# Kernel optimization log

Measured on AMD Instinct MI355X. Metric: run time of the kernel, lower is better.

The kernel has to match this reference:

```python
import jax, jax.numpy as jnp
import numpy as np

D = 256        # node/edge feature dim
H = 256        # MLP hidden dim
NG = 80000     # grid (src) nodes
NM = 20000     # mesh (dst) nodes
E = 160000     # g2m edges
EPS = 1e-5


def _mlp(x, W1, b1, W2, b2, g, beta):
    # MeshGraphMLP with hidden_layers=1: Linear -> SiLU -> Linear -> LayerNorm
    h = jax.nn.silu(x @ W1 + b1)
    y = h @ W2 + b2
    mu = jnp.mean(y, axis=-1, keepdims=True)
    var = jnp.var(y, axis=-1, keepdims=True)
    return (y - mu) * jax.lax.rsqrt(var + EPS) * g + beta


def setup_inputs() -> dict:
    key = jax.random.key(0)
    ks = jax.random.split(key, 16)

    def rn(k, shape, s=0.02):
        return jax.random.normal(k, shape, dtype=jnp.float32) * s

    inp = {
        "g2m_efeat": jax.random.normal(ks[0], (E, D), dtype=jnp.float32),
        "grid_nfeat": jax.random.normal(ks[1], (NG, D), dtype=jnp.float32),
        "mesh_nfeat": jax.random.normal(ks[2], (NM, D), dtype=jnp.float32),
        "src_idx": jax.random.randint(ks[3], (E,), 0, NG, dtype=jnp.int32),
        "dst_idx": jax.random.randint(ks[4], (E,), 0, NM, dtype=jnp.int32),
        # edge MLP (concat variant): input = [efeat | src_feat | dst_feat] -> 3D
        "eW1": rn(ks[5], (3 * D, H)), "eb1": jnp.zeros((H,), jnp.float32),
        "eW2": rn(ks[6], (H, D)),     "eb2": jnp.zeros((D,), jnp.float32),
        "eg": jnp.ones((D,), jnp.float32), "ebeta": jnp.zeros((D,), jnp.float32),
        # src node MLP: D -> H -> D
        "sW1": rn(ks[7], (D, H)), "sb1": jnp.zeros((H,), jnp.float32),
        "sW2": rn(ks[8], (H, D)), "sb2": jnp.zeros((D,), jnp.float32),
        "sg": jnp.ones((D,), jnp.float32), "sbeta": jnp.zeros((D,), jnp.float32),
        # dst node MLP: (D_agg + D_node) = 2D -> H -> D
        "dW1": rn(ks[9], (2 * D, H)), "db1": jnp.zeros((H,), jnp.float32),
        "dW2": rn(ks[10], (H, D)),    "db2": jnp.zeros((D,), jnp.float32),
        "dg": jnp.ones((D,), jnp.float32), "dbeta": jnp.zeros((D,), jnp.float32),
    }
    return inp


def reference(g2m_efeat, grid_nfeat, mesh_nfeat, src_idx, dst_idx,
              eW1, eb1, eW2, eb2, eg, ebeta,
              sW1, sb1, sW2, sb2, sg, sbeta,
              dW1, db1, dW2, db2, dg, dbeta):
    # edge MLP: gather src/dst node features, concat with edge features
    e_in = jnp.concatenate(
        [g2m_efeat, grid_nfeat[src_idx], mesh_nfeat[dst_idx]], axis=-1)  # [E, 3D]
    efeat = _mlp(e_in, eW1, eb1, eW2, eb2, eg, ebeta)                    # [E, D]
    # aggregate_and_concat: copy_e_sum scatter to dst mesh nodes, concat node feats
    agg = jax.ops.segment_sum(efeat, dst_idx, num_segments=NM)           # [NM, D]
    cat_feat = jnp.concatenate([agg, mesh_nfeat], axis=-1)               # [NM, 2D]
    mesh_out = mesh_nfeat + _mlp(cat_feat, dW1, db1, dW2, db2, dg, dbeta)
    grid_out = grid_nfeat + _mlp(grid_nfeat, sW1, sb1, sW2, sb2, sg, sbeta)
    return (grid_out, mesh_out)
```

## Files before the change

### kernel.cpp

```cpp
#include <hip/hip_runtime.h>
#include <hip/hip_bf16.h>

#define DD 256
#define NGN 80000
#define NMN 20000
#define NEE 160000

typedef unsigned short u16;
typedef __attribute__((ext_vector_type(8))) short s16x8;
typedef __attribute__((ext_vector_type(4))) short s16x4;
typedef __attribute__((ext_vector_type(4))) float f32x4;

__device__ __forceinline__ u16 f2bf(float f) {
  union { float f; unsigned u; } v; v.f = f;
  unsigned r = (v.u + 0x7FFFu + ((v.u >> 16) & 1u)) >> 16;
  return (u16)r;
}

__global__ void pack_weights(const float* __restrict__ W, u16* __restrict__ dst, int K) {
  int idx = blockIdx.x * 256 + threadIdx.x;
  if (idx >= K * 256) return;
  int i = idx & 7;
  int lane = (idx >> 3) & 63;
  int nt = (idx >> 9) & 15;
  int kt = idx >> 13;
  int k = kt * 32 + 4 * (lane >> 4) + (i < 4 ? i : 12 + i);
  int n = nt * 16 + (lane & 15);
  dst[idx] = f2bf(W[(size_t)k * 256 + n]);
}

__device__ __forceinline__ void stage16k(const u16* __restrict__ gsrc, u16* lds, int tid) {
  const s16x8* s = (const s16x8*)gsrc;
  s16x8* d = (s16x8*)lds;
#pragma unroll
  for (int j = 0; j < 4; ++j) d[tid + 256 * j] = s[tid + 256 * j];
}

template <int MODE, int K1>
__global__ __launch_bounds__(256, 2) void mlp_fused(
    const float* __restrict__ xa, const float* __restrict__ xb,
    const float* __restrict__ xc,
    const int* __restrict__ sidx, const int* __restrict__ didx,
    const u16* __restrict__ W1p, const float* __restrict__ b1,
    const u16* __restrict__ W2p, const float* __restrict__ b2,
    const float* __restrict__ gam, const float* __restrict__ bet,
    const float* __restrict__ resid, float* __restrict__ out, int nrows) {
  __shared__ u16 bstage[8192];
  __shared__ u16 hbuf[64 * 256];
  __shared__ float2 pstats[64][2];

  const int tid = threadIdx.x;
  const int lane = tid & 63;
  const int wave = tid >> 6;
  const int mr = wave >> 1, nc = wave & 1;
  const int g = lane >> 4, lr = lane & 15;
  const int row0 = blockIdx.x * 64;

  const float* pA[2][3];
#pragma unroll
  for (int mt = 0; mt < 2; ++mt) {
    int r = row0 + mr * 32 + mt * 16 + lr;
    if (MODE == 2) r = min(r, nrows - 1);
    pA[mt][0] = xa + (size_t)r * DD;
    if constexpr (MODE == 0) {
      pA[mt][1] = xb + (size_t)sidx[r] * DD;
      pA[mt][2] = xc + (size_t)didx[r] * DD;
    } else if constexpr (MODE == 2) {
      pA[mt][1] = xb + (size_t)r * DD;
    }
  }

  const f32x4 fz = {0.f, 0.f, 0.f, 0.f};
  f32x4 acc[2][8];
#pragma unroll
  for (int mt = 0; mt < 2; ++mt)
#pragma unroll
    for (int nt = 0; nt < 8; ++nt) acc[mt][nt] = fz;

#pragma unroll
  for (int region = 0; region < K1 / 256; ++region) {
    for (int kl = 0; kl < 8; ++kl) {
      const int kt = region * 8 + kl;
      __syncthreads();
      stage16k(W1p + (size_t)kt * 8192, bstage, tid);
      __syncthreads();
      s16x8 afr[2];
      const int c0 = kl * 32 + 4 * g;
#pragma unroll
      for (int mt = 0; mt < 2; ++mt) {
        const float* p = pA[mt][region] + c0;
        f32x4 f0 = *(const f32x4*)p;
        f32x4 f1 = *(const f32x4*)(p + 16);
        s16x8 a;
#pragma unroll
        for (int j = 0; j < 4; ++j) {
          a[j] = (short)f2bf(f0[j]);
          a[4 + j] = (short)f2bf(f1[j]);
        }
        afr[mt] = a;
      }
#pragma unroll
      for (int nt = 0; nt < 8; ++nt) {
        s16x8 b = *(const s16x8*)(bstage + ((size_t)(nc * 8 + nt) * 64 + lane) * 8);
        acc[0][nt] = __builtin_amdgcn_mfma_f32_16x16x32_bf16(afr[0], b, acc[0][nt], 0, 0, 0);
        acc[1][nt] = __builtin_amdgcn_mfma_f32_16x16x32_bf16(afr[1], b, acc[1][nt], 0, 0, 0);
      }
    }
  }

  {
    float b1v[8];
#pragma unroll
    for (int nt = 0; nt < 8; ++nt) b1v[nt] = b1[nc * 128 + nt * 16 + lr];
#pragma unroll
    for (int mt = 0; mt < 2; ++mt)
#pragma unroll
      for (int nt = 0; nt < 8; ++nt)
#pragma unroll
        for (int i = 0; i < 4; ++i) {
          float x = acc[mt][nt][i] + b1v[nt];
          float h = x / (1.f + __expf(-x));
          int rowL = mr * 32 + mt * 16 + 4 * g + i;
          int col = nc * 128 + nt * 16 + lr;
          int byte = rowL * 512 + ((col * 2) ^ ((rowL & 7) << 4));
          *(u16*)((char*)hbuf + byte) = f2bf(h);
        }
  }

  f32x4 acc2[2][8];
#pragma unroll
  for (int mt = 0; mt < 2; ++mt)
#pragma unroll
    for (int nt = 0; nt < 8; ++nt) acc2[mt][nt] = fz;

  for (int kt2 = 0; kt2 < 8; ++kt2) {
    __syncthreads();
    stage16k(W2p + (size_t)kt2 * 8192, bstage, tid);
    __syncthreads();
    s16x8 afr[2];
#pragma unroll
    for (int mt = 0; mt < 2; ++mt) {
      int rowL = mr * 32 + mt * 16 + lr;
      int swz = (rowL & 7) << 4;
      int cL = kt2 * 32 + 4 * g;
      s16x4 lo = *(const s16x4*)((char*)hbuf + rowL * 512 + ((cL * 2) ^ swz));
      s16x4 hi = *(const s16x4*)((char*)hbuf + rowL * 512 + (((cL + 16) * 2) ^ swz));
      s16x8 a;
#pragma unroll
      for (int j = 0; j < 4; ++j) {
        a[j] = lo[j];
        a[4 + j] = hi[j];
      }
      afr[mt] = a;
    }
#pragma unroll
    for (int nt = 0; nt < 8; ++nt) {
      s16x8 b = *(const s16x8*)(bstage + ((size_t)(nc * 8 + nt) * 64 + lane) * 8);
      acc2[0][nt] = __builtin_amdgcn_mfma_f32_16x16x32_bf16(afr[0], b, acc2[0][nt], 0, 0, 0);
      acc2[1][nt] = __builtin_amdgcn_mfma_f32_16x16x32_bf16(afr[1], b, acc2[1][nt], 0, 0, 0);
    }
  }

  float b2v[8], gv[8], bv[8];
#pragma unroll
  for (int nt = 0; nt < 8; ++nt) {
    int col = nc * 128 + nt * 16 + lr;
    b2v[nt] = b2[col];
    gv[nt] = gam[col];
    bv[nt] = bet[col];
  }
#pragma unroll
  for (int mt = 0; mt < 2; ++mt)
#pragma unroll
    for (int i = 0; i < 4; ++i) {
      float s = 0.f, s2 = 0.f;
#pragma unroll
      for (int nt = 0; nt < 8; ++nt) {
        float y = acc2[mt][nt][i] + b2v[nt];
        s += y;
        s2 += y * y;
      }
#pragma unroll
      for (int m = 1; m < 16; m <<= 1) {
        s += __shfl_xor(s, m);
        s2 += __shfl_xor(s2, m);
      }
      if (lr == 0) pstats[mr * 32 + mt * 16 + 4 * g + i][nc] = make_float2(s, s2);
    }
  __syncthreads();
#pragma unroll
  for (int mt = 0; mt < 2; ++mt)
#pragma unroll
    for (int i = 0; i < 4; ++i) {
      int rowL = mr * 32 + mt * 16 + 4 * g + i;
      float2 pa = pstats[rowL][0], pb = pstats[rowL][1];
      float sum = pa.x + pb.x, sq = pa.y + pb.y;
      float mu = sum * (1.f / 256.f);
      float var = fmaxf(sq * (1.f / 256.f) - mu * mu, 0.f);
      float rs = rsqrtf(var + 1e-5f);
      int rg = row0 + rowL;
      if (MODE == 2 && rg >= nrows) continue;
      int dn = 0;
      if constexpr (MODE == 0) dn = didx[rg];
#pragma unroll
      for (int nt = 0; nt < 8; ++nt) {
        int col = nc * 128 + nt * 16 + lr;
        float y = acc2[mt][nt][i] + b2v[nt];
        float val = (y - mu) * rs * gv[nt] + bv[nt];
        if constexpr (MODE == 0) {
          atomicAdd(out + (size_t)dn * DD + col, val);
        } else {
          out[(size_t)rg * DD + col] = resid[(size_t)rg * DD + col] + val;
        }
      }
    }
}

extern "C" void kernel_launch(void* const* d_in, const int* in_sizes, int n_in,
                              void* d_out, int out_size, void* d_ws, size_t ws_size,
                              hipStream_t stream) {
  const float* g2m  = (const float*)d_in[0];
  const float* grid = (const float*)d_in[1];
  const float* mesh = (const float*)d_in[2];
  const int* sidx = (const int*)d_in[3];
  const int* didx = (const int*)d_in[4];
  const float* eW1 = (const float*)d_in[5];
  const float* eb1 = (const float*)d_in[6];
  const float* eW2 = (const float*)d_in[7];
  const float* eb2 = (const float*)d_in[8];
  const float* eg  = (const float*)d_in[9];
  const float* ebt = (const float*)d_in[10];
  const float* sW1 = (const float*)d_in[11];
  const float* sb1 = (const float*)d_in[12];
  const float* sW2 = (const float*)d_in[13];
  const float* sb2 = (const float*)d_in[14];
  const float* sg  = (const float*)d_in[15];
  const float* sbt = (const float*)d_in[16];
  const float* dW1 = (const float*)d_in[17];
  const float* db1 = (const float*)d_in[18];
  const float* dW2 = (const float*)d_in[19];
  const float* db2 = (const float*)d_in[20];
  const float* dg  = (const float*)d_in[21];
  const float* dbt = (const float*)d_in[22];

  float* agg = (float*)d_ws;
  u16* wp = (u16*)((char*)d_ws + (size_t)NMN * DD * 4);
  u16* eW1p = wp;
  u16* eW2p = eW1p + 768 * 256;
  u16* sW1p = eW2p + 256 * 256;
  u16* sW2p = sW1p + 256 * 256;
  u16* dW1p = sW2p + 256 * 256;
  u16* dW2p = dW1p + 512 * 256;

  (void)hipMemsetAsync(agg, 0, (size_t)NMN * DD * 4, stream);
  pack_weights<<<768, 256, 0, stream>>>(eW1, eW1p, 768);
  pack_weights<<<256, 256, 0, stream>>>(eW2, eW2p, 256);
  pack_weights<<<256, 256, 0, stream>>>(sW1, sW1p, 256);
  pack_weights<<<256, 256, 0, stream>>>(sW2, sW2p, 256);
  pack_weights<<<512, 256, 0, stream>>>(dW1, dW1p, 512);
  pack_weights<<<256, 256, 0, stream>>>(dW2, dW2p, 256);

  float* gout = (float*)d_out;
  float* mout = gout + (size_t)NGN * DD;

  mlp_fused<0, 768><<<NEE / 64, 256, 0, stream>>>(
      g2m, grid, mesh, sidx, didx, eW1p, eb1, eW2p, eb2, eg, ebt, nullptr, agg, NEE);
  mlp_fused<1, 256><<<NGN / 64, 256, 0, stream>>>(
      grid, nullptr, nullptr, nullptr, nullptr, sW1p, sb1, sW2p, sb2, sg, sbt, grid, gout, NGN);
  mlp_fused<2, 512><<<(NMN + 63) / 64, 256, 0, stream>>>(
      agg, mesh, nullptr, nullptr, nullptr, dW1p, db1, dW2p, db2, dg, dbt, mesh, mout, NMN);
}
```

Measured before the change: 438.8 us.

## Precompute per-node projections of edge first layer instead of per-edge gathers

Splits the edge MLP's first linear layer by linearity: the grid and mesh node features are each multiplied once by their slice of W1, stored as bf16 in the output buffer as scratch, and then gathered and summed per edge. The edge kernel then only does a K=256 GEMM on edge features on top of the gathered sum, instead of a K=768 GEMM over gathered rows. Kernel order is changed so the mesh and grid MLPs run after the edge kernel and overwrite the scratch. Storing the projections in bf16 adds rounding error, and the gathers now read half-width rows.

```diff
diff --git a/kernel.cpp b/kernel.cpp
--- a/kernel.cpp
+++ b/kernel.cpp
@@ -15,6 +15,10 @@
   union { float f; unsigned u; } v; v.f = f;
   unsigned r = (v.u + 0x7FFFu + ((v.u >> 16) & 1u)) >> 16;
   return (u16)r;
+}
+__device__ __forceinline__ float bf2f(u16 x) {
+  union { unsigned u; float f; } v; v.u = ((unsigned)x) << 16;
+  return v.f;
 }
 
 __global__ void pack_weights(const float* __restrict__ W, u16* __restrict__ dst, int K) {
@@ -36,11 +40,265 @@
   for (int j = 0; j < 4; ++j) d[tid + 256 * j] = s[tid + 256 * j];
 }
 
+__global__ __launch_bounds__(256, 2) void gemm_ns(
+    const float* __restrict__ X, const u16* __restrict__ Wp,
+    u16* __restrict__ Y, int n) {
+  __shared__ u16 bstage[8192];
+  __shared__ u16 ob[16384];
+  const int tid = threadIdx.x;
+  const int lane = tid & 63;
+  const int wave = tid >> 6;
+  const int mr = wave >> 1, nc = wave & 1;
+  const int g = lane >> 4, lr = lane & 15;
+  const int row0 = blockIdx.x * 64;
+
+  const float* pX[2];
+#pragma unroll
+  for (int mt = 0; mt < 2; ++mt) {
+    int r = min(row0 + mr * 32 + mt * 16 + lr, n - 1);
+    pX[mt] = X + (size_t)r * DD;
+  }
+  const f32x4 fz = {0.f, 0.f, 0.f, 0.f};
+  f32x4 acc[2][8];
+#pragma unroll
+  for (int mt = 0; mt < 2; ++mt)
+#pragma unroll
+    for (int nt = 0; nt < 8; ++nt) acc[mt][nt] = fz;
+
+  for (int kl = 0; kl < 8; ++kl) {
+    __syncthreads();
+    stage16k(Wp + (size_t)kl * 8192, bstage, tid);
+    __syncthreads();
+    s16x8 afr[2];
+    const int c0 = kl * 32 + 4 * g;
+#pragma unroll
+    for (int mt = 0; mt < 2; ++mt) {
+      f32x4 f0 = *(const f32x4*)(pX[mt] + c0);
+      f32x4 f1 = *(const f32x4*)(pX[mt] + c0 + 16);
+      s16x8 a;
+#pragma unroll
+      for (int j = 0; j < 4; ++j) {
+        a[j] = (short)f2bf(f0[j]);
+        a[4 + j] = (short)f2bf(f1[j]);
+      }
+      afr[mt] = a;
+    }
+#pragma unroll
+    for (int nt = 0; nt < 8; ++nt) {
+      s16x8 b = *(const s16x8*)(bstage + ((size_t)(nc * 8 + nt) * 64 + lane) * 8);
+      acc[0][nt] = __builtin_amdgcn_mfma_f32_16x16x32_bf16(afr[0], b, acc[0][nt], 0, 0, 0);
+      acc[1][nt] = __builtin_amdgcn_mfma_f32_16x16x32_bf16(afr[1], b, acc[1][nt], 0, 0, 0);
+    }
+  }
+#pragma unroll
+  for (int mt = 0; mt < 2; ++mt)
+#pragma unroll
+    for (int nt = 0; nt < 8; ++nt)
+#pragma unroll
+      for (int i = 0; i < 4; ++i) {
+        int rowL = mr * 32 + mt * 16 + 4 * g + i;
+        int col = nc * 128 + nt * 16 + lr;
+        int byte = rowL * 512 + ((col * 2) ^ ((rowL & 7) << 4));
+        *(u16*)((char*)ob + byte) = f2bf(acc[mt][nt][i]);
+      }
+  __syncthreads();
+#pragma unroll
+  for (int rr = 0; rr < 16; ++rr) {
+    int rowL = wave * 16 + rr;
+    int rg = row0 + rowL;
+    if (rg < n) {
+      s16x4 v = *(const s16x4*)((char*)ob + rowL * 512 + ((lane * 8) ^ ((rowL & 7) << 4)));
+      *(s16x4*)(Y + (size_t)rg * DD + lane * 4) = v;
+    }
+  }
+}
+
+__global__ __launch_bounds__(256, 2) void edge_fused(
+    const float* __restrict__ efeat,
+    const u16* __restrict__ GSp, const u16* __restrict__ GMp,
+    const int* __restrict__ sidx, const int* __restrict__ didx,
+    const u16* __restrict__ W1p, const float* __restrict__ b1,
+    const u16* __restrict__ W2p, const float* __restrict__ b2,
+    const float* __restrict__ gam, const float* __restrict__ bet,
+    float* __restrict__ agg) {
+  __shared__ u16 uni[16384];
+  __shared__ u16 bstage[8192];
+  __shared__ float2 pstats[64][2];
+
+  const int tid = threadIdx.x;
+  const int lane = tid & 63;
+  const int wave = tid >> 6;
+  const int mr = wave >> 1, nc = wave & 1;
+  const int g = lane >> 4, lr = lane & 15;
+  const int row0 = blockIdx.x * 64;
+
+#pragma unroll
+  for (int j = 0; j < 8; ++j) {
+    int e = wave * 16 + j * 2 + (lane >> 5);
+    int rg = row0 + e;
+    int rs = sidx[rg], rd = didx[rg];
+    int co = (lane & 31) * 8;
+    s16x8 a = *(const s16x8*)(GSp + (size_t)rs * DD + co);
+    s16x8 b = *(const s16x8*)(GMp + (size_t)rd * DD + co);
+    s16x8 o;
+#pragma unroll
+    for (int k2 = 0; k2 < 8; ++k2)
+      o[k2] = (short)f2bf(bf2f((u16)a[k2]) + bf2f((u16)b[k2]));
+    int byte = e * 512 + ((co * 2) ^ ((e & 7) << 4));
+    *(s16x8*)((char*)uni + byte) = o;
+  }
+  __syncthreads();
+
+  f32x4 acc[2][8];
+#pragma unroll
+  for (int mt = 0; mt < 2; ++mt)
+#pragma unroll
+    for (int nt = 0; nt < 8; ++nt)
+#pragma unroll
+      for (int i = 0; i < 4; ++i) {
+        int rowL = mr * 32 + mt * 16 + 4 * g + i;
+        int col = nc * 128 + nt * 16 + lr;
+        int byte = rowL * 512 + ((col * 2) ^ ((rowL & 7) << 4));
+        acc[mt][nt][i] = bf2f(*(const u16*)((char*)uni + byte));
+      }
+
+  const float* pe[2];
+#pragma unroll
+  for (int mt = 0; mt < 2; ++mt)
+    pe[mt] = efeat + (size_t)(row0 + mr * 32 + mt * 16 + lr) * DD;
+
+  for (int kl = 0; kl < 8; ++kl) {
+    __syncthreads();
+    stage16k(W1p + (size_t)kl * 8192, bstage, tid);
+    __syncthreads();
+    s16x8 afr[2];
+    const int c0 = kl * 32 + 4 * g;
+#pragma unroll
+    for (int mt = 0; mt < 2; ++mt) {
+      f32x4 f0 = *(const f32x4*)(pe[mt] + c0);
+      f32x4 f1 = *(const f32x4*)(pe[mt] + c0 + 16);
+      s16x8 a;
+#pragma unroll
+      for (int j = 0; j < 4; ++j) {
+        a[j] = (short)f2bf(f0[j]);
+        a[4 + j] = (short)f2bf(f1[j]);
+      }
+      afr[mt] = a;
+    }
+#pragma unroll
+    for (int nt = 0; nt < 8; ++nt) {
+      s16x8 b = *(const s16x8*)(bstage + ((size_t)(nc * 8 + nt) * 64 + lane) * 8);
+      acc[0][nt] = __builtin_amdgcn_mfma_f32_16x16x32_bf16(afr[0], b, acc[0][nt], 0, 0, 0);
+      acc[1][nt] = __builtin_amdgcn_mfma_f32_16x16x32_bf16(afr[1], b, acc[1][nt], 0, 0, 0);
+    }
+  }
+
+  {
+    float b1v[8];
+#pragma unroll
+    for (int nt = 0; nt < 8; ++nt) b1v[nt] = b1[nc * 128 + nt * 16 + lr];
+#pragma unroll
+    for (int mt = 0; mt < 2; ++mt)
+#pragma unroll
+      for (int nt = 0; nt < 8; ++nt)
+#pragma unroll
+        for (int i = 0; i < 4; ++i) {
+          float x = acc[mt][nt][i] + b1v[nt];
+          float h = x / (1.f + __expf(-x));
+          int rowL = mr * 32 + mt * 16 + 4 * g + i;
+          int col = nc * 128 + nt * 16 + lr;
+          int byte = rowL * 512 + ((col * 2) ^ ((rowL & 7) << 4));
+          *(u16*)((char*)uni + byte) = f2bf(h);
+        }
+  }
+
+  f32x4 acc2[2][8];
+  const f32x4 fz = {0.f, 0.f, 0.f, 0.f};
+#pragma unroll
+  for (int mt = 0; mt < 2; ++mt)
+#pragma unroll
+    for (int nt = 0; nt < 8; ++nt) acc2[mt][nt] = fz;
+
+  for (int kt2 = 0; kt2 < 8; ++kt2) {
+    __syncthreads();
+    stage16k(W2p + (size_t)kt2 * 8192, bstage, tid);
+    __syncthreads();
+    s16x8 afr[2];
+#pragma unroll
+    for (int mt = 0; mt < 2; ++mt) {
+      int rowL = mr * 32 + mt * 16 + lr;
+      int swz = (rowL & 7) << 4;
+      int cL = kt2 * 32 + 4 * g;
+      s16x4 lo = *(const s16x4*)((char*)uni + rowL * 512 + ((cL * 2) ^ swz));
+      s16x4 hi = *(const s16x4*)((char*)uni + rowL * 512 + (((cL + 16) * 2) ^ swz));
+      s16x8 a;
+#pragma unroll
+      for (int j = 0; j < 4; ++j) {
+        a[j] = lo[j];
+        a[4 + j] = hi[j];
+      }
+      afr[mt] = a;
+    }
+#pragma unroll
+    for (int nt = 0; nt < 8; ++nt) {
+      s16x8 b = *(const s16x8*)(bstage + ((size_t)(nc * 8 + nt) * 64 + lane) * 8);
+      acc2[0][nt] = __builtin_amdgcn_mfma_f32_16x16x32_bf16(afr[0], b, acc2[0][nt], 0, 0, 0);
+      acc2[1][nt] = __builtin_amdgcn_mfma_f32_16x16x32_bf16(afr[1], b, acc2[1][nt], 0, 0, 0);
+    }
+  }
+
+  float b2v[8], gv[8], bv[8];
+#pragma unroll
+  for (int nt = 0; nt < 8; ++nt) {
+    int col = nc * 128 + nt * 16 + lr;
+    b2v[nt] = b2[col];
+    gv[nt] = gam[col];
+    bv[nt] = bet[col];
+  }
+#pragma unroll
+  for (int mt = 0; mt < 2; ++mt)
+#pragma unroll
+    for (int i = 0; i < 4; ++i) {
+      float s = 0.f, s2 = 0.f;
+#pragma unroll
+      for (int nt = 0; nt < 8; ++nt) {
+        float y = acc2[mt][nt][i] + b2v[nt];
+        s += y;
+        s2 += y * y;
+      }
+#pragma unroll
+      for (int m = 1; m < 16; m <<= 1) {
+        s += __shfl_xor(s, m);
+        s2 += __shfl_xor(s2, m);
+      }
+      if (lr == 0) pstats[mr * 32 + mt * 16 + 4 * g + i][nc] = make_float2(s, s2);
+    }
+  __syncthreads();
+#pragma unroll
+  for (int mt = 0; mt < 2; ++mt)
+#pragma unroll
+    for (int i = 0; i < 4; ++i) {
+      int rowL = mr * 32 + mt * 16 + 4 * g + i;
+      float2 pa = pstats[rowL][0], pb = pstats[rowL][1];
+      float sum = pa.x + pb.x, sq = pa.y + pb.y;
+      float mu = sum * (1.f / 256.f);
+      float var = fmaxf(sq * (1.f / 256.f) - mu * mu, 0.f);
+      float rs = rsqrtf(var + 1e-5f);
+      int rg = row0 + rowL;
+      int dn = didx[rg];
+#pragma unroll
+      for (int nt = 0; nt < 8; ++nt) {
+        int col = nc * 128 + nt * 16 + lr;
+        float y = acc2[mt][nt][i] + b2v[nt];
+        float val = (y - mu) * rs * gv[nt] + bv[nt];
+        atomicAdd(agg + (size_t)dn * DD + col, val);
+      }
+    }
+}
+
 template <int MODE, int K1>
 __global__ __launch_bounds__(256, 2) void mlp_fused(
     const float* __restrict__ xa, const float* __restrict__ xb,
-    const float* __restrict__ xc,
-    const int* __restrict__ sidx, const int* __restrict__ didx,
     const u16* __restrict__ W1p, const float* __restrict__ b1,
     const u16* __restrict__ W2p, const float* __restrict__ b2,
     const float* __restrict__ gam, const float* __restrict__ bet,
@@ -56,18 +314,13 @@
   const int g = lane >> 4, lr = lane & 15;
   const int row0 = blockIdx.x * 64;
 
-  const float* pA[2][3];
+  const float* pA[2][2];
 #pragma unroll
   for (int mt = 0; mt < 2; ++mt) {
     int r = row0 + mr * 32 + mt * 16 + lr;
     if (MODE == 2) r = min(r, nrows - 1);
     pA[mt][0] = xa + (size_t)r * DD;
-    if constexpr (MODE == 0) {
-      pA[mt][1] = xb + (size_t)sidx[r] * DD;
-      pA[mt][2] = xc + (size_t)didx[r] * DD;
-    } else if constexpr (MODE == 2) {
-      pA[mt][1] = xb + (size_t)r * DD;
-    }
+    if constexpr (MODE == 2) pA[mt][1] = xb + (size_t)r * DD;
   }
 
   const f32x4 fz = {0.f, 0.f, 0.f, 0.f};
@@ -200,18 +453,12 @@
       float rs = rsqrtf(var + 1e-5f);
       int rg = row0 + rowL;
       if (MODE == 2 && rg >= nrows) continue;
-      int dn = 0;
-      if constexpr (MODE == 0) dn = didx[rg];
 #pragma unroll
       for (int nt = 0; nt < 8; ++nt) {
         int col = nc * 128 + nt * 16 + lr;
         float y = acc2[mt][nt][i] + b2v[nt];
         float val = (y - mu) * rs * gv[nt] + bv[nt];
-        if constexpr (MODE == 0) {
-          atomicAdd(out + (size_t)dn * DD + col, val);
-        } else {
-          out[(size_t)rg * DD + col] = resid[(size_t)rg * DD + col] + val;
-        }
+        out[(size_t)rg * DD + col] = resid[(size_t)rg * DD + col] + val;
       }
     }
 }
@@ -252,6 +499,11 @@
   u16* dW1p = sW2p + 256 * 256;
   u16* dW2p = dW1p + 512 * 256;
 
+  float* gout = (float*)d_out;
+  float* mout = gout + (size_t)NGN * DD;
+  u16* GSp = (u16*)d_out;
+  u16* GMp = GSp + (size_t)NGN * DD;
+
   (void)hipMemsetAsync(agg, 0, (size_t)NMN * DD * 4, stream);
   pack_weights<<<768, 256, 0, stream>>>(eW1, eW1p, 768);
   pack_weights<<<256, 256, 0, stream>>>(eW2, eW2p, 256);
@@ -260,13 +512,14 @@
   pack_weights<<<512, 256, 0, stream>>>(dW1, dW1p, 512);
   pack_weights<<<256, 256, 0, stream>>>(dW2, dW2p, 256);
 
-  float* gout = (float*)d_out;
-  float* mout = gout + (size_t)NGN * DD;
-
-  mlp_fused<0, 768><<<NEE / 64, 256, 0, stream>>>(
-      g2m, grid, mesh, sidx, didx, eW1p, eb1, eW2p, eb2, eg, ebt, nullptr, agg, NEE);
+  gemm_ns<<<NGN / 64, 256, 0, stream>>>(grid, eW1p + 8 * 8192, GSp, NGN);
+  gemm_ns<<<(NMN + 63) / 64, 256, 0, stream>>>(mesh, eW1p + 16 * 8192, GMp, NMN);
+
+  edge_fused<<<NEE / 64, 256, 0, stream>>>(
+      g2m, GSp, GMp, sidx, didx, eW1p, eb1, eW2p, eb2, eg, ebt, agg);
+
+  mlp_fused<2, 512><<<(NMN + 63) / 64, 256, 0, stream>>>(
+      agg, mesh, dW1p, db1, dW2p, db2, dg, dbt, mesh, mout, NMN);
   mlp_fused<1, 256><<<NGN / 64, 256, 0, stream>>>(
-      grid, nullptr, nullptr, nullptr, nullptr, sW1p, sb1, sW2p, sb2, sg, sbt, grid, gout, NGN);
-  mlp_fused<2, 512><<<(NMN + 63) / 64, 256, 0, stream>>>(
-      agg, mesh, nullptr, nullptr, nullptr, dW1p, db1, dW2p, db2, dg, dbt, mesh, mout, NMN);
-}
+      grid, nullptr, sW1p, sb1, sW2p, sb2, sg, sbt, grid, gout, NGN);
+}
```

Measured after the change: 446.9 us. No clear change (+1.8%).
